# Performance work log

Hardware: AMD Instinct MI355X
Metric: run time of the kernel (lower is better)

The kernel has to match this reference:

```python
import jax, jax.numpy as jnp
import numpy as np

NUM_FRAMES = 8
NUM_CLASSES = 40
INNER_TH = 0.5
MIN_WH = 0.05
SUPPRESS = 1e9


def _xyxy_to_cxcywh(b):
    x1, y1, x2, y2 = b[..., 0], b[..., 1], b[..., 2], b[..., 3]
    return jnp.stack([(x1 + x2) * 0.5, (y1 + y2) * 0.5, x2 - x1, y2 - y1], -1)


def setup_inputs() -> dict:
    key = jax.random.key(0)
    k1, k2, k3, k4, k5 = jax.random.split(key, 5)
    B, N, T = 4, 20, NUM_FRAMES
    H = W = 160
    # valid xyxy boxes: centers in [0.1,0.9], wh in [0.02,0.3]
    c = jax.random.uniform(k1, (B, N, T, 2), minval=0.1, maxval=0.9)
    wh = jax.random.uniform(k2, (B, N, T, 2), minval=0.02, maxval=0.3)
    gt_boxes = jnp.concatenate([c - wh / 2, c + wh / 2], -1).astype(jnp.float32)
    gt_labels = jax.random.randint(k3, (B, N), 0, NUM_CLASSES)
    ids = jax.random.randint(k4, (B, N, T), 0, 100)
    drop = jax.random.bernoulli(k5, 0.1, (B, N, T))
    gt_ids = jnp.where(drop, -1, ids)  # -1 => instance absent in that frame
    ys, xs = jnp.meshgrid(jnp.arange(H), jnp.arange(W), indexing='ij')
    ref_points = jnp.stack([(xs.reshape(-1) + 0.5) / W, (ys.reshape(-1) + 0.5) / H], -1).astype(jnp.float32)
    spatial_shapes = jnp.array([H, W], dtype=jnp.int32)
    return dict(gt_labels=gt_labels, gt_boxes=gt_boxes, gt_ids=gt_ids,
                ref_points=ref_points, spatial_shapes=spatial_shapes)


def _match_frame(dist_t, ids_t, labels, valid):
    # dist_t [N,P], ids_t [N], labels [N], valid [N]; sequential suppression over n
    N, P = dist_t.shape
    arangeP = jnp.arange(P)
    arangeC = jnp.arange(NUM_CLASSES)

    def step(carry, n):
        d_all, ml, md, mi = carry
        d = d_all[n]                                   # [P]
        act = valid[n] & (ids_t[n] != -1)
        inner = d < INNER_TH
        # if no inner point, claim just the single closest point
        pos = jnp.where(inner.any(), inner, arangeP == jnp.argmin(d)) & act
        lab = labels[n]
        score = 1.0 - 2.0 * jnp.clip(d, 0.0, INNER_TH)
        ml = jnp.where(pos, lab, ml)
        md = jnp.where(pos[:, None] & (arangeC == lab)[None, :], score[:, None], md)
        mi = jnp.where(pos, ids_t[n], mi)
        d_all = jnp.where(pos[None, :], SUPPRESS, d_all)  # suppress claimed points for all gts
        return (d_all, ml, md, mi), None

    init = (dist_t,
            jnp.full((P,), -1, jnp.int32),
            jnp.zeros((P, NUM_CLASSES), dist_t.dtype),
            jnp.full((P,), -1, jnp.int32))
    (_, ml, md, mi), _ = jax.lax.scan(step, init, jnp.arange(N))
    return ml, md, mi


def reference(gt_labels, gt_boxes, gt_ids, ref_points, spatial_shapes):
    B, N, T, _ = gt_boxes.shape
    boxes_c = _xyxy_to_cxcywh(gt_boxes)                 # [B,N,T,4]
    area = (boxes_c[..., 2] * boxes_c[..., 3]).mean(-1)  # [B,N] mean area over frames
    order = jnp.argsort(area, axis=1)                   # process small instances first
    boxes_c = jnp.take_along_axis(boxes_c, order[:, :, None, None], axis=1)
    labels = jnp.take_along_axis(gt_labels.astype(jnp.int32), order, axis=1)
    ids = jnp.take_along_axis(gt_ids.astype(jnp.int32), order[:, :, None], axis=1)
    valid = (boxes_c[..., 2:] > 0.0).all(-1).any(-1) & (labels >= 0)  # [B,N]
    # normalized center distance: [B,N,T,P]
    diff = (boxes_c[..., None, :2] - ref_points[None, None, None, :, :]) / jnp.clip(boxes_c[..., None, 2:], MIN_WH)
    dist = jnp.sum(diff ** 2, -1)
    f = jax.vmap(jax.vmap(_match_frame, in_axes=(1, 1, None, None)), in_axes=(0, 0, 0, 0))
    ml, md, mi = f(dist, ids, labels, valid)            # [B,T,P], [B,T,P,C], [B,T,P]
    return ml, md, mi
```

## Files before the change

### kernel.cpp

```cpp
#include <hip/hip_runtime.h>

#define BB   4
#define NGT  20
#define TT   8
#define PP   25600
#define CC   40
#define TPB  1024
#define SUPP 1e9f
#define INNER_TH 0.5f
#define FILLB 224

#define PK_CLAIM  1u
#define PK_LAB_SH 1
#define PK_ID_SH  7
#define PK_MDV    (1u << 14)
#define PK_MDC_SH 15
#define PK_MDN_SH 21

__device__ inline unsigned long long shfl_down_u64(unsigned long long v, int off) {
    unsigned lo = (unsigned)v, hi = (unsigned)(v >> 32);
    lo = __shfl_down(lo, off, 64);
    hi = __shfl_down(hi, off, 64);
    return ((unsigned long long)hi << 32) | (unsigned long long)lo;
}

__device__ inline float4 make_geo(const float* __restrict__ gt_boxes, int b, int n, int t) {
    const float* bx = gt_boxes + ((size_t)(b * NGT + n) * TT + t) * 4;
    float x1 = bx[0], y1 = bx[1], x2 = bx[2], y2 = bx[3];
    float4 g;
    g.x = __fmul_rn(__fadd_rn(x1, x2), 0.5f);
    g.y = __fmul_rn(__fadd_rn(y1, y2), 0.5f);
    g.z = fmaxf(__fsub_rn(x2, x1), 0.05f);
    g.w = fmaxf(__fsub_rn(y2, y1), 0.05f);
    return g;
}

__device__ inline float point_dist(int px, int py, float4 g) {
    float rxv = __fdiv_rn((float)px + 0.5f, 160.0f);
    float ryv = __fdiv_rn((float)py + 0.5f, 160.0f);
    float dx = __fdiv_rn(__fsub_rn(g.x, rxv), g.z);
    float dy = __fdiv_rn(__fsub_rn(g.y, ryv), g.w);
    return __fadd_rn(__fmul_rn(dx, dx), __fmul_rn(dy, dy));
}

__global__ __launch_bounds__(TPB) void match_fill_kernel(
        const int*   __restrict__ gt_labels,
        const float* __restrict__ gt_boxes,
        const int*   __restrict__ gt_ids,
        unsigned* __restrict__ packs_g,
        uint4*    __restrict__ md4) {
    if (blockIdx.x >= BB * TT) {
        const int MD4 = BB * TT * PP * CC / 4;
        const int stride = FILLB * TPB;
        uint4 z = make_uint4(0u, 0u, 0u, 0u);
        for (int i = (blockIdx.x - BB * TT) * TPB + (int)threadIdx.x; i < MD4; i += stride)
            md4[i] = z;
        return;
    }

    int bt = blockIdx.x;
    int b  = bt >> 3;
    int t  = bt & 7;
    int tid = threadIdx.x;

    __shared__ unsigned s_pack[PP];
    __shared__ unsigned s_mask[160 * 5];
    __shared__ float  s_dxx[NGT * 160];
    __shared__ float  s_dyy[NGT * 160];
    __shared__ float  s_area[NGT];
    __shared__ int    s_valid[NGT];
    __shared__ int    s_order[NGT];
    __shared__ int    s_any[NGT];
    __shared__ float4 s_geo[NGT];
    __shared__ int4   s_meta[NGT];
    __shared__ int    s_actlist[NGT];
    __shared__ int    s_actcnt;
    __shared__ unsigned long long s_wave[TPB / 64];
    __shared__ unsigned long long s_bcast;

    {
        uint4 z = make_uint4(0u, 0u, 0u, 0u);
        for (int i = tid; i < PP / 4; i += TPB) ((uint4*)s_pack)[i] = z;
    }
    if (tid < 160 * 5) s_mask[tid] = 0u;
    if (tid < NGT) {
        const float* bx = gt_boxes + (size_t)(b * NGT + tid) * TT * 4;
        float a[TT];
        int anyPos = 0;
        for (int f = 0; f < TT; f++) {
            float w = __fsub_rn(bx[f * 4 + 2], bx[f * 4 + 0]);
            float h = __fsub_rn(bx[f * 4 + 3], bx[f * 4 + 1]);
            a[f] = __fmul_rn(w, h);
            anyPos |= (w > 0.0f && h > 0.0f) ? 1 : 0;
        }
        float s = __fadd_rn(__fadd_rn(__fadd_rn(a[0], a[1]), __fadd_rn(a[2], a[3])),
                            __fadd_rn(__fadd_rn(a[4], a[5]), __fadd_rn(a[6], a[7])));
        s_area[tid]  = __fmul_rn(s, 0.125f);
        s_valid[tid] = (anyPos && gt_labels[b * NGT + tid] >= 0) ? 1 : 0;
        s_any[tid]   = 0;
    }
    __syncthreads();

    if (tid < NGT) {
        float an = s_area[tid];
        int r = 0;
        for (int m2 = 0; m2 < NGT; m2++) {
            float am = s_area[m2];
            r += (am < an || (am == an && m2 < tid)) ? 1 : 0;
        }
        s_order[r] = tid;
    }
    __syncthreads();

    if (tid < NGT) {
        int n   = s_order[tid];
        int src = b * NGT + n;
        s_geo[tid] = make_geo(gt_boxes, b, n, t);
        int id = gt_ids[src * TT + t];
        int4 mm;
        mm.x = gt_labels[src];
        mm.y = id;
        mm.z = (s_valid[n] && id != -1) ? 1 : 0;
        mm.w = n;
        s_meta[tid] = mm;
    }
    __syncthreads();
    if (tid == 0) {
        int c = 0;
        for (int k = 0; k < NGT; k++)
            if (s_meta[k].z) s_actlist[c++] = k;
        s_actcnt = c;
    }

    for (int i = tid; i < NGT * 320; i += TPB) {
        int slot = i / 320;
        int w    = i - slot * 320;
        float4 g = s_geo[slot];
        if (w < 160) {
            float rxv = __fdiv_rn((float)w + 0.5f, 160.0f);
            float dx  = __fdiv_rn(__fsub_rn(g.x, rxv), g.z);
            s_dxx[slot * 160 + w] = __fmul_rn(dx, dx);
        } else {
            int py = w - 160;
            float ryv = __fdiv_rn((float)py + 0.5f, 160.0f);
            float dy  = __fdiv_rn(__fsub_rn(g.y, ryv), g.w);
            s_dyy[slot * 160 + py] = __fmul_rn(dy, dy);
        }
    }
    __syncthreads();
    int actcnt = s_actcnt;

    for (int j = 0; j < actcnt; j++) {
        int slot = s_actlist[j];
        int4 m  = s_meta[slot];
        float4 g = s_geo[slot];
        const float* dxx = s_dxx + slot * 160;
        const float* dyy = s_dyy + slot * 160;

        float ex = __fmul_rn(g.z, 0.70711f);
        float ey = __fmul_rn(g.w, 0.70711f);
        int x0 = max(0,   (int)floorf((g.x - ex) * 160.0f - 0.5f) - 1);
        int x1 = min(159, (int)ceilf ((g.x + ex) * 160.0f - 0.5f) + 1);
        int y0 = max(0,   (int)floorf((g.y - ey) * 160.0f - 0.5f) - 1);
        int y1 = min(159, (int)ceilf ((g.y + ey) * 160.0f - 0.5f) + 1);
        int rw = x1 - x0 + 1;
        int M  = rw * (y1 - y0 + 1);

        unsigned base = PK_CLAIM | ((unsigned)m.x << PK_LAB_SH) |
                        ((unsigned)m.y << PK_ID_SH) | PK_MDV |
                        ((unsigned)m.x << PK_MDC_SH) |
                        ((unsigned)m.w << PK_MDN_SH);
        int found = 0;
        {
            int r  = tid / rw;
            int c  = tid - r * rw;
            int dr = TPB / rw;
            int dc = TPB - dr * rw;
            for (int i = tid; i < M; i += TPB) {
                int px = x0 + c;
                int py = y0 + r;
                int p  = py * 160 + px;
                if (!(s_pack[p] & PK_CLAIM)) {
                    float d = __fadd_rn(dxx[px], dyy[py]);
                    if (d < INNER_TH) {
                        s_pack[p] = base;
                        atomicOr(&s_mask[p >> 5], 1u << (p & 31));
                        found = 1;
                    }
                }
                c += dc; r += dr;
                if (c >= rw) { c -= rw; r++; }
            }
        }
        if (found) s_any[j] = 1;
        __syncthreads();

        if (!s_any[j]) {
            unsigned long long key = ~0ULL;
            if (tid < 160) {
                int y = tid;
                unsigned um[5];
#pragma unroll
                for (int w = 0; w < 5; w++) um[w] = ~s_mask[y * 5 + w];
                unsigned anyu = um[0] | um[1] | um[2] | um[3] | um[4];
                if (!anyu) {
                    if (y == 0)
                        key = ((unsigned long long)__float_as_uint(SUPP) << 32);
                } else {
                    float dyyv = dyy[y];
                    int xs = (int)floorf(__fsub_rn(__fmul_rn(g.x, 160.0f), 0.5f));
                    xs = min(max(xs, -2), 161);
                    float bd = 2e9f;
                    int   bx = -1;
#pragma unroll
                    for (int k2 = 0; k2 < 2; k2++) {
                        int x = xs + k2;
                        if (x >= 0 && x <= 159 && ((um[x >> 5] >> (x & 31)) & 1u)) {
                            float d2 = __fadd_rn(dxx[x], dyyv);
                            if (d2 < bd || (d2 == bd && x < bx)) { bd = d2; bx = x; }
                        }
                    }
                    {
                        int xq = min(xs - 1, 159);
                        int xL = -1;
                        if (xq >= 0) {
                            int w = xq >> 5;
                            unsigned mm = um[w] & (0xffffffffu >> (31 - (xq & 31)));
                            while (true) {
                                if (mm) { xL = (w << 5) + (31 - __clz(mm)); break; }
                                if (--w < 0) break;
                                mm = um[w];
                            }
                        }
                        if (xL >= 0) {
                            float dL = __fadd_rn(dxx[xL], dyyv);
                            while (xL > 0) {
                                int xq2 = xL - 1;
                                int w = xq2 >> 5;
                                unsigned mm = um[w] & (0xffffffffu >> (31 - (xq2 & 31)));
                                int x2 = -1;
                                while (true) {
                                    if (mm) { x2 = (w << 5) + (31 - __clz(mm)); break; }
                                    if (--w < 0) break;
                                    mm = um[w];
                                }
                                if (x2 < 0) break;
                                if (__fadd_rn(dxx[x2], dyyv) != dL) break;
                                xL = x2;
                            }
                            if (dL < bd || (dL == bd && xL < bx)) { bd = dL; bx = xL; }
                        }
                    }
                    {
                        int xq = max(xs + 2, 0);
                        int xR = -1;
                        if (xq <= 159) {
                            int w = xq >> 5;
                            unsigned mm = um[w] & (0xffffffffu << (xq & 31));
                            while (true) {
                                if (mm) { xR = (w << 5) + (__ffs(mm) - 1); break; }
                                if (++w > 4) break;
                                mm = um[w];
                            }
                        }
                        if (xR >= 0) {
                            float dR = __fadd_rn(dxx[xR], dyyv);
                            if (dR < bd || (dR == bd && xR < bx)) { bd = dR; bx = xR; }
                        }
                    }
                    if (bx >= 0) {
                        int p = y * 160 + bx;
                        key = ((unsigned long long)__float_as_uint(bd) << 32) |
                              (unsigned long long)(unsigned)p;
                    }
                }
            }
            unsigned long long v = key;
            for (int off = 32; off > 0; off >>= 1) {
                unsigned long long o = shfl_down_u64(v, off);
                v = (o < v) ? o : v;
            }
            int lane = tid & 63, wave = tid >> 6;
            if (lane == 0) s_wave[wave] = v;
            __syncthreads();
            if (tid == 0) {
                unsigned long long mval = s_wave[0];
                for (int w = 1; w < TPB / 64; w++) mval = (s_wave[w] < mval) ? s_wave[w] : mval;
                s_bcast = mval;
            }
            __syncthreads();
            unsigned long long gmin = s_bcast;
            float minv = __uint_as_float((unsigned)(gmin >> 32));
            int minp = (int)(unsigned)(gmin & 0xffffffffu);
            if ((minp & (TPB - 1)) == tid) {
                unsigned npk = PK_CLAIM | ((unsigned)m.x << PK_LAB_SH) |
                               ((unsigned)m.y << PK_ID_SH);
                if (minv < SUPP) {
                    s_pack[minp] = npk;
                } else {
                    unsigned old = s_pack[minp];
                    unsigned mdbits = old & (PK_MDV | (63u << PK_MDC_SH) | (31u << PK_MDN_SH));
                    if ((old & PK_MDV) &&
                        ((old >> PK_MDC_SH) & 63u) == (unsigned)m.x) mdbits = 0u;
                    s_pack[minp] = npk | mdbits;
                }
                atomicOr(&s_mask[minp >> 5], 1u << (minp & 31));
            }
            __syncthreads();
        }
    }

    __syncthreads();
    uint4* dst = (uint4*)(packs_g + (size_t)bt * PP);
    for (int i = tid; i < PP / 4; i += TPB) dst[i] = ((const uint4*)s_pack)[i];
}

__global__ __launch_bounds__(256) void scatter_kernel(
        const unsigned* __restrict__ packs,
        const float*    __restrict__ gt_boxes,
        float* __restrict__ out) {
    const int    ML = BB * TT * PP;
    const size_t MD = (size_t)BB * TT * PP * CC;
    int f = blockIdx.x * 256 + threadIdx.x;
    uint4 pk4 = ((const uint4*)packs)[f];

    float4 vml, vmi;
    vml.x = (pk4.x & PK_CLAIM) ? (float)((pk4.x >> PK_LAB_SH) & 63u) : -1.0f;
    vml.y = (pk4.y & PK_CLAIM) ? (float)((pk4.y >> PK_LAB_SH) & 63u) : -1.0f;
    vml.z = (pk4.z & PK_CLAIM) ? (float)((pk4.z >> PK_LAB_SH) & 63u) : -1.0f;
    vml.w = (pk4.w & PK_CLAIM) ? (float)((pk4.w >> PK_LAB_SH) & 63u) : -1.0f;
    vmi.x = (pk4.x & PK_CLAIM) ? (float)((pk4.x >> PK_ID_SH) & 127u) : -1.0f;
    vmi.y = (pk4.y & PK_CLAIM) ? (float)((pk4.y >> PK_ID_SH) & 127u) : -1.0f;
    vmi.z = (pk4.z & PK_CLAIM) ? (float)((pk4.z >> PK_ID_SH) & 127u) : -1.0f;
    vmi.w = (pk4.w & PK_CLAIM) ? (float)((pk4.w >> PK_ID_SH) & 127u) : -1.0f;
    ((float4*)out)[f] = vml;
    ((float4*)(out + ML + MD))[f] = vmi;

    int pt0 = f << 2;
#pragma unroll
    for (int k = 0; k < 4; k++) {
        unsigned pk = (k == 0) ? pk4.x : (k == 1) ? pk4.y : (k == 2) ? pk4.z : pk4.w;
        if (pk & PK_MDV) {
            int pt  = pt0 + k;
            int cls = (int)((pk >> PK_MDC_SH) & 63u);
            int n   = (int)((pk >> PK_MDN_SH) & 31u);
            int bt  = pt / PP;
            int p   = pt - bt * PP;
            int py  = p / 160;
            int px  = p - py * 160;
            float4 g = make_geo(gt_boxes, bt >> 3, n, bt & 7);
            float d  = point_dist(px, py, g);
            out[ML + (size_t)pt * CC + cls] = __fsub_rn(1.0f, __fmul_rn(2.0f, d));
        }
    }
}

extern "C" void kernel_launch(void* const* d_in, const int* in_sizes, int n_in,
                              void* d_out, int out_size, void* d_ws, size_t ws_size,
                              hipStream_t stream) {
    const int*   gt_labels = (const int*)d_in[0];
    const float* gt_boxes  = (const float*)d_in[1];
    const int*   gt_ids    = (const int*)d_in[2];

    unsigned* packs = (unsigned*)d_ws;
    float*    outf  = (float*)d_out;

    match_fill_kernel<<<BB * TT + FILLB, TPB, 0, stream>>>(
        gt_labels, gt_boxes, gt_ids, packs,
        (uint4*)(outf + BB * TT * PP));

    scatter_kernel<<<(BB * TT * PP / 4) / 256, 256, 0, stream>>>(packs, gt_boxes, outf);
}
```

Baseline: 165.3 us.

## Run sequential GT suppression loop in a single wavefront; use nontemporal zero-fill stores

Moves the per-GT sequential claim/suppression loop from the full 1024-thread block into one 64-lane wavefront, replacing block-wide __syncthreads and the cross-wave min reduction with wave barriers, __any, and shuffle reductions. Drops a block barrier by recomputing box geometry from global memory in the distance precompute. Zero-fill of the big one-hot output now uses nontemporal stores. The trade is less parallelism per GT box (64 lanes scan the region instead of 1024) in exchange for far fewer block-wide barriers.

```diff
diff --git a/kernel.cpp b/kernel.cpp
--- a/kernel.cpp
+++ b/kernel.cpp
@@ -17,6 +17,8 @@
 #define PK_MDC_SH 15
 #define PK_MDN_SH 21
 
+typedef unsigned uv4 __attribute__((ext_vector_type(4)));
+
 __device__ inline unsigned long long shfl_down_u64(unsigned long long v, int off) {
     unsigned lo = (unsigned)v, hi = (unsigned)(v >> 32);
     lo = __shfl_down(lo, off, 64);
@@ -52,9 +54,10 @@
     if (blockIdx.x >= BB * TT) {
         const int MD4 = BB * TT * PP * CC / 4;
         const int stride = FILLB * TPB;
-        uint4 z = make_uint4(0u, 0u, 0u, 0u);
+        uv4 z = {0u, 0u, 0u, 0u};
+        uv4* dst = (uv4*)md4;
         for (int i = (blockIdx.x - BB * TT) * TPB + (int)threadIdx.x; i < MD4; i += stride)
-            md4[i] = z;
+            __builtin_nontemporal_store(z, dst + i);
         return;
     }
 
@@ -70,13 +73,10 @@
     __shared__ float  s_area[NGT];
     __shared__ int    s_valid[NGT];
     __shared__ int    s_order[NGT];
-    __shared__ int    s_any[NGT];
     __shared__ float4 s_geo[NGT];
     __shared__ int4   s_meta[NGT];
     __shared__ int    s_actlist[NGT];
     __shared__ int    s_actcnt;
-    __shared__ unsigned long long s_wave[TPB / 64];
-    __shared__ unsigned long long s_bcast;
 
     {
         uint4 z = make_uint4(0u, 0u, 0u, 0u);
@@ -97,7 +97,6 @@
                             __fadd_rn(__fadd_rn(a[4], a[5]), __fadd_rn(a[6], a[7])));
         s_area[tid]  = __fmul_rn(s, 0.125f);
         s_valid[tid] = (anyPos && gt_labels[b * NGT + tid] >= 0) ? 1 : 0;
-        s_any[tid]   = 0;
     }
     __syncthreads();
 
@@ -124,18 +123,17 @@
         mm.w = n;
         s_meta[tid] = mm;
     }
-    __syncthreads();
     if (tid == 0) {
         int c = 0;
         for (int k = 0; k < NGT; k++)
             if (s_meta[k].z) s_actlist[c++] = k;
         s_actcnt = c;
     }
-
     for (int i = tid; i < NGT * 320; i += TPB) {
         int slot = i / 320;
         int w    = i - slot * 320;
-        float4 g = s_geo[slot];
+        int n    = s_order[slot];
+        float4 g = make_geo(gt_boxes, b, n, t);
         if (w < 160) {
             float rxv = __fdiv_rn((float)w + 0.5f, 160.0f);
             float dx  = __fdiv_rn(__fsub_rn(g.x, rxv), g.z);
@@ -148,65 +146,68 @@
         }
     }
     __syncthreads();
-    int actcnt = s_actcnt;
-
-    for (int j = 0; j < actcnt; j++) {
-        int slot = s_actlist[j];
-        int4 m  = s_meta[slot];
-        float4 g = s_geo[slot];
-        const float* dxx = s_dxx + slot * 160;
-        const float* dyy = s_dyy + slot * 160;
-
-        float ex = __fmul_rn(g.z, 0.70711f);
-        float ey = __fmul_rn(g.w, 0.70711f);
-        int x0 = max(0,   (int)floorf((g.x - ex) * 160.0f - 0.5f) - 1);
-        int x1 = min(159, (int)ceilf ((g.x + ex) * 160.0f - 0.5f) + 1);
-        int y0 = max(0,   (int)floorf((g.y - ey) * 160.0f - 0.5f) - 1);
-        int y1 = min(159, (int)ceilf ((g.y + ey) * 160.0f - 0.5f) + 1);
-        int rw = x1 - x0 + 1;
-        int M  = rw * (y1 - y0 + 1);
-
-        unsigned base = PK_CLAIM | ((unsigned)m.x << PK_LAB_SH) |
-                        ((unsigned)m.y << PK_ID_SH) | PK_MDV |
-                        ((unsigned)m.x << PK_MDC_SH) |
-                        ((unsigned)m.w << PK_MDN_SH);
-        int found = 0;
-        {
-            int r  = tid / rw;
-            int c  = tid - r * rw;
-            int dr = TPB / rw;
-            int dc = TPB - dr * rw;
-            for (int i = tid; i < M; i += TPB) {
-                int px = x0 + c;
-                int py = y0 + r;
-                int p  = py * 160 + px;
-                if (!(s_pack[p] & PK_CLAIM)) {
-                    float d = __fadd_rn(dxx[px], dyy[py]);
-                    if (d < INNER_TH) {
-                        s_pack[p] = base;
-                        atomicOr(&s_mask[p >> 5], 1u << (p & 31));
-                        found = 1;
-                    }
+
+    if (tid < 64) {
+        int actcnt = s_actcnt;
+        for (int j = 0; j < actcnt; j++) {
+            int slot = s_actlist[j];
+            int4 m  = s_meta[slot];
+            float4 g = s_geo[slot];
+            const float* dxx = s_dxx + slot * 160;
+            const float* dyy = s_dyy + slot * 160;
+
+            float ex = __fmul_rn(g.z, 0.70711f);
+            float ey = __fmul_rn(g.w, 0.70711f);
+            int x0 = max(0,   (int)floorf((g.x - ex) * 160.0f - 0.5f) - 1);
+            int x1 = min(159, (int)ceilf ((g.x + ex) * 160.0f - 0.5f) + 1);
+            int y0 = max(0,   (int)floorf((g.y - ey) * 160.0f - 0.5f) - 1);
+            int y1 = min(159, (int)ceilf ((g.y + ey) * 160.0f - 0.5f) + 1);
+            int rw = x1 - x0 + 1;
+            int M  = rw * (y1 - y0 + 1);
+
+            unsigned base = PK_CLAIM | ((unsigned)m.x << PK_LAB_SH) |
+                            ((unsigned)m.y << PK_ID_SH) | PK_MDV |
+                            ((unsigned)m.x << PK_MDC_SH) |
+                            ((unsigned)m.w << PK_MDN_SH);
+            int found = 0;
+            {
+                int r  = tid / rw;
+                int c  = tid - r * rw;
+                int dr = 64 / rw;
+                int dc = 64 - dr * rw;
+                for (int i = tid; i < M; i += 64) {
+                    int px = x0 + c;
+                    int py = y0 + r;
+                    int p  = py * 160 + px;
+                    if (!(s_pack[p] & PK_CLAIM)) {
+                        float d = __fadd_rn(dxx[px], dyy[py]);
+                        if (d < INNER_TH) {
+                            s_pack[p] = base;
+                            atomicOr(&s_mask[p >> 5], 1u << (p & 31));
+                            found = 1;
+                        }
+                    }
+                    c += dc; r += dr;
+                    if (c >= rw) { c -= rw; r++; }
                 }
-                c += dc; r += dr;
-                if (c >= rw) { c -= rw; r++; }
             }
-        }
-        if (found) s_any[j] = 1;
-        __syncthreads();
-
-        if (!s_any[j]) {
-            unsigned long long key = ~0ULL;
-            if (tid < 160) {
-                int y = tid;
-                unsigned um[5];
+            __builtin_amdgcn_wave_barrier();
+
+            if (!__any(found)) {
+                unsigned long long key = ~0ULL;
+                for (int y = tid; y < 160; y += 64) {
+                    unsigned um[5];
 #pragma unroll
-                for (int w = 0; w < 5; w++) um[w] = ~s_mask[y * 5 + w];
-                unsigned anyu = um[0] | um[1] | um[2] | um[3] | um[4];
-                if (!anyu) {
-                    if (y == 0)
-                        key = ((unsigned long long)__float_as_uint(SUPP) << 32);
-                } else {
+                    for (int w = 0; w < 5; w++) um[w] = ~s_mask[y * 5 + w];
+                    unsigned anyu = um[0] | um[1] | um[2] | um[3] | um[4];
+                    if (!anyu) {
+                        if (y == 0) {
+                            unsigned long long kk =
+                                ((unsigned long long)__float_as_uint(SUPP) << 32);
+                            key = (kk < key) ? kk : key;
+                        }
+                        continue;
+                    }
                     float dyyv = dyy[y];
                     int xs = (int)floorf(__fsub_rn(__fmul_rn(g.x, 160.0f), 0.5f));
                     xs = min(max(xs, -2), 161);
@@ -270,47 +271,40 @@
                     }
                     if (bx >= 0) {
                         int p = y * 160 + bx;
-                        key = ((unsigned long long)__float_as_uint(bd) << 32) |
-                              (unsigned long long)(unsigned)p;
+                        unsigned long long kk =
+                            ((unsigned long long)__float_as_uint(bd) << 32) |
+                            (unsigned long long)(unsigned)p;
+                        key = (kk < key) ? kk : key;
                     }
                 }
+                unsigned long long v = key;
+                for (int off = 32; off > 0; off >>= 1) {
+                    unsigned long long o = shfl_down_u64(v, off);
+                    v = (o < v) ? o : v;
+                }
+                if (tid == 0) {
+                    float minv = __uint_as_float((unsigned)(v >> 32));
+                    int minp = (int)(unsigned)(v & 0xffffffffu);
+                    unsigned npk = PK_CLAIM | ((unsigned)m.x << PK_LAB_SH) |
+                                   ((unsigned)m.y << PK_ID_SH);
+                    if (minv < SUPP) {
+                        s_pack[minp] = npk;
+                    } else {
+                        unsigned old = s_pack[minp];
+                        unsigned mdbits = old & (PK_MDV | (63u << PK_MDC_SH) |
+                                                 (31u << PK_MDN_SH));
+                        if ((old & PK_MDV) &&
+                            ((old >> PK_MDC_SH) & 63u) == (unsigned)m.x) mdbits = 0u;
+                        s_pack[minp] = npk | mdbits;
+                    }
+                    s_mask[minp >> 5] |= 1u << (minp & 31);
+                }
+                __builtin_amdgcn_wave_barrier();
             }
-            unsigned long long v = key;
-            for (int off = 32; off > 0; off >>= 1) {
-                unsigned long long o = shfl_down_u64(v, off);
-                v = (o < v) ? o : v;
-            }
-            int lane = tid & 63, wave = tid >> 6;
-            if (lane == 0) s_wave[wave] = v;
-            __syncthreads();
-            if (tid == 0) {
-                unsigned long long mval = s_wave[0];
-                for (int w = 1; w < TPB / 64; w++) mval = (s_wave[w] < mval) ? s_wave[w] : mval;
-                s_bcast = mval;
-            }
-            __syncthreads();
-            unsigned long long gmin = s_bcast;
-            float minv = __uint_as_float((unsigned)(gmin >> 32));
-            int minp = (int)(unsigned)(gmin & 0xffffffffu);
-            if ((minp & (TPB - 1)) == tid) {
-                unsigned npk = PK_CLAIM | ((unsigned)m.x << PK_LAB_SH) |
-                               ((unsigned)m.y << PK_ID_SH);
-                if (minv < SUPP) {
-                    s_pack[minp] = npk;
-                } else {
-                    unsigned old = s_pack[minp];
-                    unsigned mdbits = old & (PK_MDV | (63u << PK_MDC_SH) | (31u << PK_MDN_SH));
-                    if ((old & PK_MDV) &&
-                        ((old >> PK_MDC_SH) & 63u) == (unsigned)m.x) mdbits = 0u;
-                    s_pack[minp] = npk | mdbits;
-                }
-                atomicOr(&s_mask[minp >> 5], 1u << (minp & 31));
-            }
-            __syncthreads();
-        }
-    }
-
+        }
+    }
     __syncthreads();
+
     uint4* dst = (uint4*)(packs_g + (size_t)bt * PP);
     for (int i = tid; i < PP / 4; i += TPB) dst[i] = ((const uint4*)s_pack)[i];
 }
```

Result: slower. 289.9 us (+75.4%).
